# Kernel tuning notes

Measured on AMD Instinct MI355X. Metric: run time of the kernel, lower is better.

Reference implementation:

```python
import jax, jax.numpy as jnp
import numpy as np

B, H, W, C = 32, 56, 56, 384
HEADS, WIN, SHIFT = 12, 7, 3
MLP_HID = 4 * C
N = WIN * WIN
EPS = 1e-5


def _rel_pos_index(win):
    ch, cw = np.meshgrid(np.arange(win), np.arange(win), indexing='ij')
    coords = np.stack([ch.ravel(), cw.ravel()])            # (2, N)
    rel = coords[:, :, None] - coords[:, None, :]          # (2, N, N)
    rel = rel.transpose(1, 2, 0).astype(np.int64)
    rel[:, :, 0] += win - 1
    rel[:, :, 1] += win - 1
    rel[:, :, 0] *= 2 * win - 1
    return rel.sum(-1)                                     # (N, N)


def _attn_mask(Hh, Ww, win, shift):
    img = np.zeros((Hh, Ww))
    cnt = 0
    slices = (slice(0, -win), slice(-win, -shift), slice(-shift, None))
    for hs in slices:
        for ws in slices:
            img[hs, ws] = cnt
            cnt += 1
    m = img.reshape(Hh // win, win, Ww // win, win).transpose(0, 2, 1, 3).reshape(-1, win * win)
    am = m[:, None, :] - m[:, :, None]
    return np.where(am != 0, -100.0, 0.0).astype(np.float32)  # (nW, N, N)


REL_IDX = jnp.asarray(_rel_pos_index(WIN))
ATTN_MASK = jnp.asarray(_attn_mask(H, W, WIN, SHIFT))


def setup_inputs() -> dict:
    key = jax.random.key(0)
    ks = jax.random.split(key, 16)
    s = 0.02
    return {
        'x': jax.random.normal(ks[0], (B, H * W, C), jnp.float32),
        'g1': jnp.ones((C,), jnp.float32),
        'b1': jnp.zeros((C,), jnp.float32),
        'qkv_w': jax.random.normal(ks[1], (3 * C, C), jnp.float32) * s,
        'qkv_b': jnp.zeros((3 * C,), jnp.float32),
        'rel_bias': jax.random.normal(ks[2], ((2 * WIN - 1) ** 2, HEADS), jnp.float32) * s,
        'proj_w': jax.random.normal(ks[3], (C, C), jnp.float32) * s,
        'proj_b': jnp.zeros((C,), jnp.float32),
        'g2': jnp.ones((C,), jnp.float32),
        'b2': jnp.zeros((C,), jnp.float32),
        'fc1_w': jax.random.normal(ks[4], (MLP_HID, C), jnp.float32) * s,
        'fc1_b': jnp.zeros((MLP_HID,), jnp.float32),
        'fc2_w': jax.random.normal(ks[5], (C, MLP_HID), jnp.float32) * s,
        'fc2_b': jnp.zeros((C,), jnp.float32),
    }


def _ln(x, g, b):
    m = x.mean(-1, keepdims=True)
    v = jnp.var(x, axis=-1, keepdims=True)
    return (x - m) * jax.lax.rsqrt(v + EPS) * g + b


def reference(x, g1, b1, qkv_w, qkv_b, rel_bias, proj_w, proj_b, g2, b2, fc1_w, fc1_b, fc2_w, fc2_b):
    Bz, L, Cc = x.shape
    hd = Cc // HEADS
    nWh = H // WIN
    shortcut = x

    h = _ln(x, g1, b1).reshape(Bz, H, W, Cc)
    h = jnp.roll(h, (-SHIFT, -SHIFT), axis=(1, 2))
    # window partition -> (Bz*nW, N, C)
    h = h.reshape(Bz, nWh, WIN, nWh, WIN, Cc).transpose(0, 1, 3, 2, 4, 5).reshape(-1, N, Cc)

    qkv = (h @ qkv_w.T + qkv_b).reshape(-1, N, 3, HEADS, hd).transpose(2, 0, 3, 1, 4)
    q, k, v = qkv[0] * (hd ** -0.5), qkv[1], qkv[2]
    attn = jnp.einsum('bhnd,bhmd->bhnm', q, k)  # (Bz*nW, heads, N, N)

    bias = rel_bias[REL_IDX.reshape(-1)].reshape(N, N, HEADS).transpose(2, 0, 1)
    attn = attn + bias[None]

    nW = ATTN_MASK.shape[0]
    attn = attn.reshape(Bz, nW, HEADS, N, N) + ATTN_MASK[None, :, None]
    attn = jax.nn.softmax(attn, axis=-1).reshape(-1, HEADS, N, N)

    out = jnp.einsum('bhnm,bhmd->bhnd', attn, v).transpose(0, 2, 1, 3).reshape(-1, N, Cc)
    out = out @ proj_w.T + proj_b
    # window reverse + unshift
    out = out.reshape(Bz, nWh, nWh, WIN, WIN, Cc).transpose(0, 1, 3, 2, 4, 5).reshape(Bz, H, W, Cc)
    out = jnp.roll(out, (SHIFT, SHIFT), axis=(1, 2)).reshape(Bz, L, Cc)

    x = shortcut + out
    h2 = _ln(x, g2, b2)
    h2 = jax.nn.gelu(h2 @ fc1_w.T + fc1_b, approximate=False)
    h2 = h2 @ fc2_w.T + fc2_b
    return x + h2
```

## Files before the change

kernel.cpp:

```cpp
#include <hip/hip_runtime.h>
#include <hip/hip_bf16.h>
#include <math.h>

#define B_      32
#define H_      56
#define W_      56
#define C_      384
#define HEADS_  12
#define WIN_    7
#define SHIFT_  3
#define NTOK_   49
#define HD_     32
#define T_      100352
#define MLP_    1536

typedef __bf16 bf16x8 __attribute__((ext_vector_type(8)));
typedef unsigned short u16x8 __attribute__((ext_vector_type(8)));
typedef float  f32x4  __attribute__((ext_vector_type(4)));

__device__ __forceinline__ float bf2f(unsigned short u) {
  union { unsigned int i; float f; } v; v.i = ((unsigned int)u) << 16; return v.f;
}
__device__ __forceinline__ unsigned short f2bf(float f) {
  union { float f; unsigned int i; } v; v.f = f;
  unsigned int x = v.i;
  return (unsigned short)((x + 0x7fffu + ((x >> 16) & 1u)) >> 16);
}
__device__ __forceinline__ float gelu_exact(float x) {
  return 0.5f * x * (1.0f + erff(x * 0.7071067811865475f));
}
__device__ __forceinline__ void gload_lds16(const void* g, void* l) {
  __builtin_amdgcn_global_load_lds(
      (const __attribute__((address_space(1))) void*)g,
      (__attribute__((address_space(3))) void*)l, 16, 0, 0);
}
__device__ __forceinline__ bf16x8 ldg8(const unsigned short* p) {
  u16x8 v = *(const u16x8*)p;
  return __builtin_bit_cast(bf16x8, v);
}

__global__ __launch_bounds__(256)
void wconv_kernel(const float* __restrict__ src, unsigned short* __restrict__ dst, int n) {
  const int i = (blockIdx.x * 256 + threadIdx.x) * 4;
  if (i < n) {
    const float4 v = *(const float4*)(src + i);
    ushort4 o;
    o.x = f2bf(v.x); o.y = f2bf(v.y); o.z = f2bf(v.z); o.w = f2bf(v.w);
    *(ushort4*)(dst + i) = o;
  }
}

template<int REMAP>
__global__ __launch_bounds__(256)
void ln_kernel(const float* __restrict__ xin, const float* __restrict__ g,
               const float* __restrict__ bb, unsigned short* __restrict__ outbf) {
  const int m = blockIdx.x * 4 + (threadIdx.x >> 6);
  const int lane = threadIdx.x & 63;
  size_t src;
  if (REMAP) {
    int w = m / NTOK_, t = m - w * NTOK_;
    int bz = w >> 6, widx = w & 63;
    int wh = widx >> 3, ww = widx & 7;
    int ih = t / WIN_, iw = t - ih * WIN_;
    int gh = (wh * WIN_ + ih + SHIFT_) % H_;
    int gw = (ww * WIN_ + iw + SHIFT_) % W_;
    src = ((size_t)bz * (H_ * W_) + gh * W_ + gw) * C_;
  } else {
    src = (size_t)m * C_;
  }
  const float* row = xin + src;
  float v[6]; float s = 0.f, s2 = 0.f;
#pragma unroll
  for (int u = 0; u < 6; ++u) {
    v[u] = row[lane + 64 * u];
    s += v[u]; s2 += v[u] * v[u];
  }
#pragma unroll
  for (int off = 32; off; off >>= 1) {
    s  += __shfl_xor(s, off);
    s2 += __shfl_xor(s2, off);
  }
  const float mean = s * (1.0f / C_);
  const float var  = s2 * (1.0f / C_) - mean * mean;
  const float rstd = rsqrtf(var + 1e-5f);
  unsigned short* orow = outbf + (size_t)m * C_;
#pragma unroll
  for (int u = 0; u < 6; ++u) {
    int c = lane + 64 * u;
    orow[c] = f2bf((v[u] - mean) * rstd * g[c] + bb[c]);
  }
}

#define BM 128
#define BN 128
#define BKg 64

template<int EPI, int BSRC>
__global__ __launch_bounds__(256)
void mfma_gemm(const unsigned short* __restrict__ A,
               const void* __restrict__ Wv,
               const float* __restrict__ bias,
               void* __restrict__ outv,
               const float* __restrict__ resid,
               int M, int Nn, int K) {
  __shared__ unsigned short Al[BM * BKg];
  __shared__ unsigned short Bl[BN * BKg];
  const int t    = threadIdx.x;
  const int wid  = t >> 6;
  const int lane = t & 63;
  const int wr   = wid >> 1, wc = wid & 1;

  const unsigned int nb = gridDim.x * gridDim.y;
  unsigned int lin = blockIdx.y * gridDim.x + blockIdx.x;
  lin = (lin & 7) * (nb >> 3) + (lin >> 3);
  const int m0 = (int)(lin / gridDim.x) * BM;
  const int n0 = (int)(lin % gridDim.x) * BN;

  f32x4 acc[4][4] = {};

  const int sr8    = lane >> 3;
  const int schunk = (lane & 7) ^ (sr8 & 7);
  const int brow   = t >> 3;
  const int bchunk = t & 7;

  const int fr  = lane & 15;
  const int fq  = lane >> 4;

  for (int k0 = 0; k0 < K; k0 += BKg) {
    __syncthreads();
#pragma unroll
    for (int i = 0; i < 4; ++i) {
      const int r = i * 32 + wid * 8 + sr8;
      gload_lds16(A + (size_t)(m0 + r) * K + k0 + schunk * 8,
                  (void*)(Al + (size_t)(i * 32 + wid * 8) * BKg));
    }
    if (BSRC == 1) {
      const unsigned short* Wb = (const unsigned short*)Wv;
#pragma unroll
      for (int i = 0; i < 4; ++i) {
        const int r = i * 32 + wid * 8 + sr8;
        gload_lds16(Wb + (size_t)(n0 + r) * K + k0 + schunk * 8,
                    (void*)(Bl + (size_t)(i * 32 + wid * 8) * BKg));
      }
    } else {
      const float* Wf = (const float*)Wv;
#pragma unroll
      for (int p = 0; p < 4; ++p) {
        const int rb = p * 32 + brow;
        const float* wp = Wf + (size_t)(n0 + rb) * K + k0 + bchunk * 8;
        const float4 w0 = *(const float4*)(wp);
        const float4 w1 = *(const float4*)(wp + 4);
        bf16x8 pv;
        pv[0] = (__bf16)w0.x; pv[1] = (__bf16)w0.y;
        pv[2] = (__bf16)w0.z; pv[3] = (__bf16)w0.w;
        pv[4] = (__bf16)w1.x; pv[5] = (__bf16)w1.y;
        pv[6] = (__bf16)w1.z; pv[7] = (__bf16)w1.w;
        const int sw = bchunk ^ (rb & 7);
        *(bf16x8*)(Bl + (size_t)rb * BKg + sw * 8) = pv;
      }
    }
    __syncthreads();

#pragma unroll
    for (int kk = 0; kk < 2; ++kk) {
      bf16x8 af[4], bfr[4];
#pragma unroll
      for (int mi = 0; mi < 4; ++mi) {
        const int row = wr * 64 + mi * 16 + fr;
        const int ch  = (kk * 4 + fq) ^ (row & 7);
        af[mi] = *(const bf16x8*)(Al + (size_t)row * BKg + ch * 8);
      }
#pragma unroll
      for (int ni = 0; ni < 4; ++ni) {
        const int row = wc * 64 + ni * 16 + fr;
        const int ch  = (kk * 4 + fq) ^ (row & 7);
        bfr[ni] = *(const bf16x8*)(Bl + (size_t)row * BKg + ch * 8);
      }
#pragma unroll
      for (int mi = 0; mi < 4; ++mi)
#pragma unroll
        for (int ni = 0; ni < 4; ++ni)
          acc[mi][ni] = __builtin_amdgcn_mfma_f32_16x16x32_bf16(
              af[mi], bfr[ni], acc[mi][ni], 0, 0, 0);
    }
  }

  const int ecol  = fr;
  const int erow0 = fq * 4;
#pragma unroll
  for (int mi = 0; mi < 4; ++mi) {
#pragma unroll
    for (int r = 0; r < 4; ++r) {
      const int m = m0 + wr * 64 + mi * 16 + erow0 + r;
      size_t dstbase = 0;
      if (EPI == 2) {
        int w = m / NTOK_, tt = m - w * NTOK_;
        int bz = w >> 6, widx = w & 63;
        int wh = widx >> 3, ww = widx & 7;
        int ih = tt / WIN_, iw = tt - ih * WIN_;
        int gh = (wh * WIN_ + ih + SHIFT_) % H_;
        int gw = (ww * WIN_ + iw + SHIFT_) % W_;
        dstbase = ((size_t)bz * (H_ * W_) + gh * W_ + gw) * C_;
      }
#pragma unroll
      for (int ni = 0; ni < 4; ++ni) {
        const int n = n0 + wc * 64 + ni * 16 + ecol;
        float val = acc[mi][ni][r] + bias[n];
        if (EPI == 0) {
          ((unsigned short*)outv)[(size_t)m * Nn + n] = f2bf(val);
        } else if (EPI == 1) {
          ((unsigned short*)outv)[(size_t)m * Nn + n] = f2bf(gelu_exact(val));
        } else if (EPI == 2) {
          ((float*)outv)[dstbase + n] = resid[dstbase + n] + val;
        } else {
          float* o = (float*)outv + (size_t)m * Nn + n;
          *o += val;
        }
      }
    }
  }
}

__global__ __launch_bounds__(64)
void bias_expand_kernel(const float* __restrict__ rel_bias,
                        float* __restrict__ biasx) {
  const int hi = blockIdx.x;
  const int head = hi / NTOK_, i = hi - head * NTOK_;
  const int j = threadIdx.x;
  if (j < NTOK_) {
    const int ih = i / 7, iw = i - ih * 7;
    const int jh = j / 7, jw = j - jh * 7;
    const int ridx = (ih - jh + 6) * 13 + (iw - jw + 6);
    biasx[(size_t)hi * NTOK_ + j] = rel_bias[ridx * HEADS_ + head];
  }
}

#define AW 2
__global__ __launch_bounds__(64 * AW)
void attn_mfma_kernel(const unsigned short* __restrict__ qkv,
                      const float* __restrict__ biasx,
                      unsigned short* __restrict__ out) {
  __shared__ unsigned short sP[AW][64 * 72];
  __shared__ unsigned short sVT[AW][32 * 72];
  const int wid  = threadIdx.x >> 6;
  const int lane = threadIdx.x & 63;
  const int task = blockIdx.x * AW + wid;
  const int w    = task / HEADS_;
  const int head = task - w * HEADS_;
  const int widx = w & 63;
  const int wh = widx >> 3, ww = widx & 7;
  const bool edge = (wh == 7) || (ww == 7);
  const int c  = lane & 15;
  const int fq = lane >> 4;
  unsigned short* Pl = sP[wid];
  unsigned short* Vl = sVT[wid];
  const unsigned short* qw = qkv + (size_t)w * NTOK_ * (3 * C_);

  u16x8 vv[4];
#pragma unroll
  for (int p = 0; p < 4; ++p)
    vv[p] = *(const u16x8*)(qw + (size_t)(p * 16 + c) * (3 * C_) + 2 * C_ + head * HD_ + fq * 8);

  bf16x8 aQ[4], bK[4];
#pragma unroll
  for (int mi = 0; mi < 4; ++mi)
    aQ[mi] = ldg8(qw + (size_t)(mi * 16 + c) * (3 * C_) + head * HD_ + fq * 8);
#pragma unroll
  for (int ni = 0; ni < 4; ++ni)
    bK[ni] = ldg8(qw + (size_t)(ni * 16 + c) * (3 * C_) + C_ + head * HD_ + fq * 8);

  const f32x4 zero4 = {0.f, 0.f, 0.f, 0.f};
  f32x4 accS[4][4];
#pragma unroll
  for (int mi = 0; mi < 4; ++mi)
#pragma unroll
    for (int ni = 0; ni < 4; ++ni)
      accS[mi][ni] = __builtin_amdgcn_mfma_f32_16x16x32_bf16(aQ[mi], bK[ni], zero4, 0, 0, 0);

#pragma unroll
  for (int p = 0; p < 4; ++p)
#pragma unroll
    for (int u = 0; u < 8; ++u)
      Vl[(fq * 8 + u) * 72 + p * 16 + c] = (unsigned short)vv[p][u];

  float rowinv[4][4];
  const float* bh = biasx + (size_t)head * (NTOK_ * NTOK_);
#pragma unroll
  for (int mi = 0; mi < 4; ++mi) {
#pragma unroll
    for (int r = 0; r < 4; ++r) {
      const int i  = mi * 16 + fq * 4 + r;
      const int ic = i < NTOK_ ? i : 0;
      const int ih = ic / 7, iw = ic - ih * 7;
      int li = 0;
      if (edge) {
        const int shi = wh * 7 + ih, swi = ww * 7 + iw;
        li = (shi < 49 ? 0 : (shi < 53 ? 1 : 2)) * 3 + (swi < 49 ? 0 : (swi < 53 ? 1 : 2));
      }
      float sv[4];
#pragma unroll
      for (int ni = 0; ni < 4; ++ni) {
        const int j  = ni * 16 + c;
        const int jc = j < NTOK_ ? j : 0;
        float s = accS[mi][ni][r] * 0.17677669529663687f + bh[ic * NTOK_ + jc];
        if (edge) {
          const int jh = jc / 7, jw = jc - jh * 7;
          const int shj = wh * 7 + jh, swj = ww * 7 + jw;
          const int lj = (shj < 49 ? 0 : (shj < 53 ? 1 : 2)) * 3 + (swj < 49 ? 0 : (swj < 53 ? 1 : 2));
          if (lj != li) s -= 100.f;
        }
        if (j >= NTOK_) s = -1e30f;
        sv[ni] = s;
      }
      float mx = fmaxf(fmaxf(sv[0], sv[1]), fmaxf(sv[2], sv[3]));
      mx = fmaxf(mx, __shfl_xor(mx, 1));
      mx = fmaxf(mx, __shfl_xor(mx, 2));
      mx = fmaxf(mx, __shfl_xor(mx, 4));
      mx = fmaxf(mx, __shfl_xor(mx, 8));
      const float e0 = __expf(sv[0] - mx), e1 = __expf(sv[1] - mx);
      const float e2 = __expf(sv[2] - mx), e3 = __expf(sv[3] - mx);
      float sm = e0 + e1 + e2 + e3;
      sm += __shfl_xor(sm, 1);
      sm += __shfl_xor(sm, 2);
      sm += __shfl_xor(sm, 4);
      sm += __shfl_xor(sm, 8);
      rowinv[mi][r] = 1.0f / sm;
      const int prow = i * 72;
      Pl[prow +  0 + c] = f2bf(e0);
      Pl[prow + 16 + c] = f2bf(e1);
      Pl[prow + 32 + c] = f2bf(e2);
      Pl[prow + 48 + c] = f2bf(e3);
    }
  }

  f32x4 accO[4][2] = {};
#pragma unroll
  for (int kk = 0; kk < 2; ++kk) {
    bf16x8 ap[4], bv[2];
#pragma unroll
    for (int mi = 0; mi < 4; ++mi)
      ap[mi] = __builtin_bit_cast(bf16x8,
          *(const u16x8*)(Pl + (mi * 16 + c) * 72 + kk * 32 + fq * 8));
#pragma unroll
    for (int nd = 0; nd < 2; ++nd)
      bv[nd] = __builtin_bit_cast(bf16x8,
          *(const u16x8*)(Vl + (nd * 16 + c) * 72 + kk * 32 + fq * 8));
#pragma unroll
    for (int mi = 0; mi < 4; ++mi)
#pragma unroll
      for (int nd = 0; nd < 2; ++nd)
        accO[mi][nd] = __builtin_amdgcn_mfma_f32_16x16x32_bf16(ap[mi], bv[nd], accO[mi][nd], 0, 0, 0);
  }

#pragma unroll
  for (int mi = 0; mi < 4; ++mi)
#pragma unroll
    for (int r = 0; r < 4; ++r) {
      const int i = mi * 16 + fq * 4 + r;
      if (i < NTOK_) {
        const float inv = rowinv[mi][r];
#pragma unroll
        for (int nd = 0; nd < 2; ++nd)
          out[(size_t)(w * NTOK_ + i) * C_ + head * HD_ + nd * 16 + c] =
              f2bf(accO[mi][nd][r] * inv);
      }
    }
}

extern "C" void kernel_launch(void* const* d_in, const int* in_sizes, int n_in,
                              void* d_out, int out_size, void* d_ws, size_t ws_size,
                              hipStream_t stream) {
  const float* x        = (const float*)d_in[0];
  const float* g1       = (const float*)d_in[1];
  const float* b1       = (const float*)d_in[2];
  const float* qkv_w    = (const float*)d_in[3];
  const float* qkv_b    = (const float*)d_in[4];
  const float* rel_bias = (const float*)d_in[5];
  const float* proj_w   = (const float*)d_in[6];
  const float* proj_b   = (const float*)d_in[7];
  const float* g2       = (const float*)d_in[8];
  const float* b2       = (const float*)d_in[9];
  const float* fc1_w    = (const float*)d_in[10];
  const float* fc1_b    = (const float*)d_in[11];
  const float* fc2_w    = (const float*)d_in[12];
  const float* fc2_b    = (const float*)d_in[13];
  float* out = (float*)d_out;

  char* ws = (char*)d_ws;
  unsigned short* xw   = (unsigned short*)(ws);
  unsigned short* qkvb = (unsigned short*)(ws + 77070336);
  unsigned short* attn_out = xw;
  unsigned short* h2   = xw;
  unsigned short* hid  = qkvb;
  unsigned short* fc2_wb  = (unsigned short*)(ws);
  unsigned short* qkv_wb  = (unsigned short*)(ws + 308412416);
  unsigned short* proj_wb = (unsigned short*)(ws + 309297152);
  float*          biasx   = (float*)(ws + 309592064);

  wconv_kernel<<<dim3(432), dim3(256), 0, stream>>>(qkv_w, qkv_wb, 3 * C_ * C_);
  wconv_kernel<<<dim3(144), dim3(256), 0, stream>>>(proj_w, proj_wb, C_ * C_);
  bias_expand_kernel<<<dim3(HEADS_ * NTOK_), dim3(64), 0, stream>>>(rel_bias, biasx);

  ln_kernel<1><<<dim3(T_ / 4), dim3(256), 0, stream>>>(x, g1, b1, xw);

  mfma_gemm<0, 1><<<dim3(1152 / BN, T_ / BM), dim3(256), 0, stream>>>(
      xw, qkv_wb, qkv_b, (void*)qkvb, nullptr, T_, 1152, 384);

  attn_mfma_kernel<<<dim3((T_ / NTOK_) * HEADS_ / AW), dim3(64 * AW), 0, stream>>>(
      qkvb, biasx, attn_out);

  mfma_gemm<2, 1><<<dim3(384 / BN, T_ / BM), dim3(256), 0, stream>>>(
      attn_out, proj_wb, proj_b, (void*)out, x, T_, 384, 384);

  ln_kernel<0><<<dim3(T_ / 4), dim3(256), 0, stream>>>(out, g2, b2, h2);

  mfma_gemm<1, 0><<<dim3(MLP_ / BN, T_ / BM), dim3(256), 0, stream>>>(
      h2, fc1_w, fc1_b, (void*)hid, nullptr, T_, MLP_, 384);

  wconv_kernel<<<dim3(576), dim3(256), 0, stream>>>(fc2_w, fc2_wb, C_ * MLP_);

  mfma_gemm<3, 1><<<dim3(384 / BN, T_ / BM), dim3(256), 0, stream>>>(
      hid, fc2_wb, fc2_b, (void*)out, nullptr, T_, 384, MLP_);
}
```

Before: 1.036 ms.

## Fuse fc1, GELU and fc2 into one MLP kernel with a tanh GELU

Replaces the separate fc1 GEMM (with GELU) and fc2 GEMM with one kernel. Each 128-row block keeps its LayerNorm-ed activations in registers and loops over 32-wide hidden chunks, staging fc1 and fc2 weight slices in LDS, so the large bf16 hidden tensor is never written to or read back from global memory. fc1 weights are now pre-converted to bf16 alongside fc2, and the exact erf GELU is swapped for a tanh approximation built on fast exp. The trade-offs are weight slices re-read by every block, two block-wide barriers per chunk that cut MFMA utilisation, and a small numerical deviation from the exact GELU.

```diff
diff --git a/kernel.cpp b/kernel.cpp
--- a/kernel.cpp
+++ b/kernel.cpp
@@ -26,8 +26,11 @@
   unsigned int x = v.i;
   return (unsigned short)((x + 0x7fffu + ((x >> 16) & 1u)) >> 16);
 }
-__device__ __forceinline__ float gelu_exact(float x) {
-  return 0.5f * x * (1.0f + erff(x * 0.7071067811865475f));
+__device__ __forceinline__ float gelu_fast(float x) {
+  const float t = 0.79788456f * x * (1.0f + 0.044715f * x * x);
+  const float e = __expf(2.0f * t);
+  const float th = 1.0f - 2.0f / (e + 1.0f);
+  return 0.5f * x * (1.0f + th);
 }
 __device__ __forceinline__ void gload_lds16(const void* g, void* l) {
   __builtin_amdgcn_global_load_lds(
@@ -95,10 +98,10 @@
 #define BN 128
 #define BKg 64
 
-template<int EPI, int BSRC>
+template<int EPI>
 __global__ __launch_bounds__(256)
 void mfma_gemm(const unsigned short* __restrict__ A,
-               const void* __restrict__ Wv,
+               const unsigned short* __restrict__ Wb,
                const float* __restrict__ bias,
                void* __restrict__ outv,
                const float* __restrict__ resid,
@@ -120,9 +123,6 @@
 
   const int sr8    = lane >> 3;
   const int schunk = (lane & 7) ^ (sr8 & 7);
-  const int brow   = t >> 3;
-  const int bchunk = t & 7;
-
   const int fr  = lane & 15;
   const int fq  = lane >> 4;
 
@@ -133,31 +133,8 @@
       const int r = i * 32 + wid * 8 + sr8;
       gload_lds16(A + (size_t)(m0 + r) * K + k0 + schunk * 8,
                   (void*)(Al + (size_t)(i * 32 + wid * 8) * BKg));
-    }
-    if (BSRC == 1) {
-      const unsigned short* Wb = (const unsigned short*)Wv;
-#pragma unroll
-      for (int i = 0; i < 4; ++i) {
-        const int r = i * 32 + wid * 8 + sr8;
-        gload_lds16(Wb + (size_t)(n0 + r) * K + k0 + schunk * 8,
-                    (void*)(Bl + (size_t)(i * 32 + wid * 8) * BKg));
-      }
-    } else {
-      const float* Wf = (const float*)Wv;
-#pragma unroll
-      for (int p = 0; p < 4; ++p) {
-        const int rb = p * 32 + brow;
-        const float* wp = Wf + (size_t)(n0 + rb) * K + k0 + bchunk * 8;
-        const float4 w0 = *(const float4*)(wp);
-        const float4 w1 = *(const float4*)(wp + 4);
-        bf16x8 pv;
-        pv[0] = (__bf16)w0.x; pv[1] = (__bf16)w0.y;
-        pv[2] = (__bf16)w0.z; pv[3] = (__bf16)w0.w;
-        pv[4] = (__bf16)w1.x; pv[5] = (__bf16)w1.y;
-        pv[6] = (__bf16)w1.z; pv[7] = (__bf16)w1.w;
-        const int sw = bchunk ^ (rb & 7);
-        *(bf16x8*)(Bl + (size_t)rb * BKg + sw * 8) = pv;
-      }
+      gload_lds16(Wb + (size_t)(n0 + r) * K + k0 + schunk * 8,
+                  (void*)(Bl + (size_t)(i * 32 + wid * 8) * BKg));
     }
     __syncthreads();
 
@@ -208,17 +185,106 @@
         float val = acc[mi][ni][r] + bias[n];
         if (EPI == 0) {
           ((unsigned short*)outv)[(size_t)m * Nn + n] = f2bf(val);
-        } else if (EPI == 1) {
-          ((unsigned short*)outv)[(size_t)m * Nn + n] = f2bf(gelu_exact(val));
-        } else if (EPI == 2) {
+        } else {
           ((float*)outv)[dstbase + n] = resid[dstbase + n] + val;
-        } else {
-          float* o = (float*)outv + (size_t)m * Nn + n;
-          *o += val;
         }
       }
     }
   }
+}
+
+__global__ __launch_bounds__(512, 2)
+void fused_mlp_kernel(const unsigned short* __restrict__ h2,
+                      const unsigned short* __restrict__ w1b,
+                      const float* __restrict__ fc1_b,
+                      const unsigned short* __restrict__ w2b,
+                      const float* __restrict__ fc2_b,
+                      float* __restrict__ out) {
+  __shared__ unsigned short w1s[32 * 384];
+  __shared__ unsigned short w2s[384 * 32];
+  __shared__ unsigned short hidc[128 * 40];
+  const int t    = threadIdx.x;
+  const int wid  = t >> 6;
+  const int lane = t & 63;
+  const int c  = lane & 15;
+  const int fq = lane >> 4;
+  const int m0 = blockIdx.x * 128;
+
+  bf16x8 aH[12];
+#pragma unroll
+  for (int ks = 0; ks < 12; ++ks)
+    aH[ks] = ldg8(h2 + (size_t)(m0 + wid * 16 + c) * 384 + ks * 32 + fq * 8);
+
+  f32x4 oacc[8][3] = {};
+
+  for (int ck = 0; ck < 48; ++ck) {
+    __syncthreads();
+#pragma unroll
+    for (int ii = 0; ii < 3; ++ii) {
+      const int i   = wid * 3 + ii;
+      const int byt = i * 1024 + lane * 16;
+      const int row = byt / 768;
+      const int rc  = (byt - row * 768) >> 4;
+      gload_lds16(w1b + (size_t)(ck * 32 + row) * 384 + ((rc ^ (row & 7)) * 8),
+                  (void*)(w1s + i * 512));
+    }
+#pragma unroll
+    for (int ii = 0; ii < 3; ++ii) {
+      const int i   = wid * 3 + ii;
+      const int row = i * 16 + (lane >> 2);
+      const int cd  = lane & 3;
+      gload_lds16(w2b + (size_t)row * MLP_ + ck * 32 + ((cd ^ (row & 3)) * 8),
+                  (void*)(w2s + i * 512));
+    }
+    __syncthreads();
+
+    f32x4 sacc[2] = {};
+#pragma unroll
+    for (int ks = 0; ks < 12; ++ks) {
+#pragma unroll
+      for (int ni = 0; ni < 2; ++ni) {
+        const int row = ni * 16 + c;
+        const int ch  = (ks * 4 + fq) ^ (row & 7);
+        bf16x8 b = *(const bf16x8*)(w1s + row * 384 + ch * 8);
+        sacc[ni] = __builtin_amdgcn_mfma_f32_16x16x32_bf16(aH[ks], b, sacc[ni], 0, 0, 0);
+      }
+    }
+#pragma unroll
+    for (int ni = 0; ni < 2; ++ni)
+#pragma unroll
+      for (int r = 0; r < 4; ++r) {
+        const int hcol = ni * 16 + c;
+        const float v = sacc[ni][r] + fc1_b[ck * 32 + hcol];
+        hidc[(wid * 16 + fq * 4 + r) * 40 + hcol] = f2bf(gelu_fast(v));
+      }
+    __syncthreads();
+
+    bf16x8 aP[8];
+#pragma unroll
+    for (int mi = 0; mi < 8; ++mi)
+      aP[mi] = *(const bf16x8*)(hidc + (mi * 16 + c) * 40 + fq * 8);
+#pragma unroll
+    for (int nj = 0; nj < 3; ++nj) {
+      const int row = wid * 48 + nj * 16 + c;
+      const int ch  = fq ^ (row & 3);
+      bf16x8 b = *(const bf16x8*)(w2s + row * 32 + ch * 8);
+#pragma unroll
+      for (int mi = 0; mi < 8; ++mi)
+        oacc[mi][nj] = __builtin_amdgcn_mfma_f32_16x16x32_bf16(aP[mi], b, oacc[mi][nj], 0, 0, 0);
+    }
+  }
+
+#pragma unroll
+  for (int mi = 0; mi < 8; ++mi)
+#pragma unroll
+    for (int r = 0; r < 4; ++r) {
+      const int m = m0 + mi * 16 + fq * 4 + r;
+#pragma unroll
+      for (int nj = 0; nj < 3; ++nj) {
+        const int n = wid * 48 + nj * 16 + c;
+        out[(size_t)m * C_ + n] += oacc[mi][nj][r] + fc2_b[n];
+      }
+    }
 }
 
 __global__ __launch_bounds__(64)
@@ -391,34 +457,31 @@
   unsigned short* qkvb = (unsigned short*)(ws + 77070336);
   unsigned short* attn_out = xw;
   unsigned short* h2   = xw;
-  unsigned short* hid  = qkvb;
-  unsigned short* fc2_wb  = (unsigned short*)(ws);
   unsigned short* qkv_wb  = (unsigned short*)(ws + 308412416);
   unsigned short* proj_wb = (unsigned short*)(ws + 309297152);
   float*          biasx   = (float*)(ws + 309592064);
+  unsigned short* fc1_wb  = (unsigned short*)(ws + 309707312);
+  unsigned short* fc2_wb  = (unsigned short*)(ws + 310886960);
 
   wconv_kernel<<<dim3(432), dim3(256), 0, stream>>>(qkv_w, qkv_wb, 3 * C_ * C_);
   wconv_kernel<<<dim3(144), dim3(256), 0, stream>>>(proj_w, proj_wb, C_ * C_);
+  wconv_kernel<<<dim3(576), dim3(256), 0, stream>>>(fc1_w, fc1_wb, MLP_ * C_);
+  wconv_kernel<<<dim3(576), dim3(256), 0, stream>>>(fc2_w, fc2_wb, C_ * MLP_);
   bias_expand_kernel<<<dim3(HEADS_ * NTOK_), dim3(64), 0, stream>>>(rel_bias, biasx);
 
   ln_kernel<1><<<dim3(T_ / 4), dim3(256), 0, stream>>>(x, g1, b1, xw);
 
-  mfma_gemm<0, 1><<<dim3(1152 / BN, T_ / BM), dim3(256), 0, stream>>>(
+  mfma_gemm<0><<<dim3(1152 / BN, T_ / BM), dim3(256), 0, stream>>>(
       xw, qkv_wb, qkv_b, (void*)qkvb, nullptr, T_, 1152, 384);
 
   attn_mfma_kernel<<<dim3((T_ / NTOK_) * HEADS_ / AW), dim3(64 * AW), 0, stream>>>(
       qkvb, biasx, attn_out);
 
-  mfma_gemm<2, 1><<<dim3(384 / BN, T_ / BM), dim3(256), 0, stream>>>(
+  mfma_gemm<2><<<dim3(384 / BN, T_ / BM), dim3(256), 0, stream>>>(
       attn_out, proj_wb, proj_b, (void*)out, x, T_, 384, 384);
 
   ln_kernel<0><<<dim3(T_ / 4), dim3(256), 0, stream>>>(out, g2, b2, h2);
 
-  mfma_gemm<1, 0><<<dim3(MLP_ / BN, T_ / BM), dim3(256), 0, stream>>>(
-      h2, fc1_w, fc1_b, (void*)hid, nullptr, T_, MLP_, 384);
-
-  wconv_kernel<<<dim3(576), dim3(256), 0, stream>>>(fc2_w, fc2_wb, C_ * MLP_);
-
-  mfma_gemm<3, 1><<<dim3(384 / BN, T_ / BM), dim3(256), 0, stream>>>(
-      hid, fc2_wb, fc2_b, (void*)out, nullptr, T_, 384, MLP_);
-}
+  fused_mlp_kernel<<<dim3(T_ / 128), dim3(512), 0, stream>>>(
+      h2, fc1_wb, fc1_b, fc2_wb, fc2_b, out);
+}
```

Result: slower. 1.229 ms (+18.6%).
